# Kernel optimization log

Hardware: AMD Instinct MI355X
Metric: run time of the kernel (lower is better)

## Reference

```python
import jax, jax.numpy as jnp
import numpy as np

# ---- module config (from init_kwargs) ----
KERNEL_SIZE = 3
DIM = 3
HALF = KERNEL_SIZE // 2          # kernel offsets span [-HALF, HALF]
COORD_RANGE = 256                # voxel grid extent per spatial axis
NUM_BATCH = 4
N_VOXELS = 100_000
FEAT_DIM = 32
STRIDE = COORD_RANGE + 2 * HALF  # encoding stride so shifted coords fit


def _kernel_offsets():
    # All offsets of a KERNEL_SIZE^DIM kernel, centered (MinkowskiEngine-style).
    r = np.arange(-HALF, HALF + 1)
    grids = np.meshgrid(*([r] * DIM), indexing='ij')
    return jnp.asarray(np.stack([g.ravel() for g in grids], axis=1), dtype=jnp.int32)  # [K, DIM]


def setup_inputs() -> dict:
    key = jax.random.key(0)
    k1, k2, k3 = jax.random.split(key, 3)
    batch = jax.random.randint(k1, (1, N_VOXELS), 0, NUM_BATCH, dtype=jnp.int32)
    coords = jax.random.randint(k2, (3, N_VOXELS), 0, COORD_RANGE, dtype=jnp.int32)
    sparse_indices = jnp.concatenate([batch, coords], axis=0)  # [4, N]
    features = jax.random.normal(k3, (N_VOXELS, FEAT_DIM), dtype=jnp.float32)
    return {"sparse_indices": sparse_indices, "features": features}


def _kernel_map_and_out_key(sparse_indices):
    offsets = _kernel_offsets()                 # [K, 3]
    K = offsets.shape[0]
    b = sparse_indices[0].astype(jnp.int32)     # [N]
    coords = sparse_indices[1:].T.astype(jnp.int32)  # [N, 3]
    N = coords.shape[0]
    NK = N * K

    # neighbor coords per (voxel, offset); shift by HALF so values are >= 0
    nbr = coords[:, None, :] + offsets[None, :, :] + HALF     # [N, K, 3]
    S = STRIDE
    # unique integer hash of (batch, x, y, z); fits in int32 for these ranges
    enc = ((b[:, None] * S + nbr[..., 0]) * S + nbr[..., 1]) * S + nbr[..., 2]
    enc = enc.reshape(-1)                                     # [NK]

    # unique keys (sorted) + inverse map; pad to static size NK
    uniq, inv = jnp.unique(enc, return_inverse=True, size=NK, fill_value=-1)

    # reorder unique keys into first-seen order to match the dict-based reference
    first = jnp.full((NK,), NK, dtype=jnp.int32).at[inv].min(
        jnp.arange(NK, dtype=jnp.int32))
    order = jnp.argsort(first)                                # padding sorts last
    new_id = jnp.zeros((NK,), dtype=jnp.int32).at[order].set(
        jnp.arange(NK, dtype=jnp.int32))
    out_idx = new_id[inv]                                     # [NK] output index per entry

    # decode unique (first-seen ordered) keys back to spatial coords
    uo = uniq[order]
    valid = uo >= 0
    z = uo % S
    y = (uo // S) % S
    x = (uo // (S * S)) % S
    out_key = jnp.stack([x, y, z], axis=1) - HALF             # undo shift
    out_key = jnp.where(valid[:, None], out_key, -1)          # [NK, 3], padded rows = -1

    input_idx = jnp.repeat(jnp.arange(N, dtype=jnp.int32), K) # [NK]
    rel_pos = jnp.tile(jnp.arange(K, dtype=jnp.int32), N)     # [NK]
    kernel_map = jnp.stack([input_idx, out_idx, rel_pos], axis=1)  # [NK, 3]
    return kernel_map, out_key


def reference(sparse_indices, features):
    kernel_map, out_key = _kernel_map_and_out_key(sparse_indices)
    NK = kernel_map.shape[0]
    # canonical downstream use of the kernel map: gather inputs, scatter-sum to outputs
    out_feats = jax.ops.segment_sum(features[kernel_map[:, 0]],
                                    kernel_map[:, 1], num_segments=NK)
    return kernel_map, out_key, out_feats
```

## Files before the change

### kernel.cpp

```cpp
#include <hip/hip_runtime.h>
#include <stdint.h>

typedef unsigned long long u64;
typedef unsigned u32;
typedef float __attribute__((ext_vector_type(4))) f4raw;

#define K 27
#define S 258
#define ENCMAX (4 * S * S * S)

struct __align__(16) BP { u64 bits; u32 pfx; u32 pad; };

__global__ void k_mark(const int* __restrict__ si, int N, u64* __restrict__ bits) {
    int idx = blockIdx.x * blockDim.x + threadIdx.x;
    if (idx >= N * 9) return;
    int n = idx / 9, run = idx - n * 9;
    int ox = run / 3, oy = run - ox * 3;
    int b = si[n], x = si[N + n], y = si[2 * N + n], z = si[3 * N + n];
    unsigned enc0 = (unsigned)(((b * S + x + ox) * S + (y + oy)) * S + z);
    unsigned w = enc0 >> 6; int bit = enc0 & 63;
    atomicOr(&bits[w], 7ull << bit);
    if (bit > 61) atomicOr(&bits[w + 1], 7ull >> (64 - bit));
}

__global__ void s1_tilesum(const u64* __restrict__ bits, int* __restrict__ tsums) {
    __shared__ int s[256];
    int tid = threadIdx.x;
    const u64* p = bits + (size_t)blockIdx.x * 4096;
    int sum = 0;
    for (int j = tid; j < 4096; j += 256) sum += __popcll(p[j]);
    s[tid] = sum; __syncthreads();
    for (int off = 128; off > 0; off >>= 1) {
        if (tid < off) s[tid] += s[tid + off];
        __syncthreads();
    }
    if (tid == 0) tsums[blockIdx.x] = s[0];
}

__global__ void k_scanB(int* __restrict__ a, int n) {
    __shared__ int s[1024];
    int tid = threadIdx.x;
    int v = (tid < n) ? a[tid] : 0;
    s[tid] = v; __syncthreads();
    for (int off = 1; off < 1024; off <<= 1) {
        int t = (tid >= off) ? s[tid - off] : 0;
        __syncthreads();
        s[tid] += t;
        __syncthreads();
    }
    if (tid == 1023) a[n] = s[1023];
    if (tid < n) a[tid] = s[tid] - v;
}

__global__ void s3_wprefix(const u64* __restrict__ bits, const int* __restrict__ tsums,
                           BP* __restrict__ bpx) {
    __shared__ int s[256];
    int tid = threadIdx.x;
    size_t base = (size_t)blockIdx.x * 4096 + (size_t)tid * 16;
    u64 wv[16]; int pc[16]; int tsum = 0;
#pragma unroll
    for (int j = 0; j < 16; j++) {
        wv[j] = bits[base + j];
        pc[j] = __popcll(wv[j]);
        tsum += pc[j];
    }
    s[tid] = tsum; __syncthreads();
    for (int off = 1; off < 256; off <<= 1) {
        int t = (tid >= off) ? s[tid - off] : 0;
        __syncthreads();
        s[tid] += t;
        __syncthreads();
    }
    int run = tsums[blockIdx.x] + s[tid] - tsum;
#pragma unroll
    for (int j = 0; j < 16; j++) {
        BP r; r.bits = wv[j]; r.pfx = (u32)run; r.pad = 0;
        bpx[base + j] = r;
        run += pc[j];
    }
}

__global__ void k_kid(const int* __restrict__ si, int N,
                      const BP* __restrict__ bpx,
                      int* __restrict__ kid, int* __restrict__ minE) {
    int idx = blockIdx.x * blockDim.x + threadIdx.x;
    if (idx >= N * 9) return;
    int n = idx / 9, run = idx - n * 9;
    int ox = run / 3, oy = run - ox * 3;
    int b = si[n], x = si[N + n], y = si[2 * N + n], z = si[3 * N + n];
    unsigned enc0 = (unsigned)(((b * S + x + ox) * S + (y + oy)) * S + z);
    int e0 = n * K + run * 3;
    unsigned w = enc0 >> 6; int bit = enc0 & 63;
    BP r = bpx[w];
    int kd0 = (int)r.pfx + __popcll(r.bits & ((1ull << bit) - 1));
    kid[e0 + 0] = kd0;
    kid[e0 + 1] = kd0 + 1;
    kid[e0 + 2] = kd0 + 2;
    atomicMin(&minE[kd0 + 0], e0 + 0);
    atomicMin(&minE[kd0 + 1], e0 + 1);
    atomicMin(&minE[kd0 + 2], e0 + 2);
}

__global__ void k_flagsum(const int* __restrict__ kid, const int* __restrict__ minE,
                          int NK, u32* __restrict__ multibk,
                          u64* __restrict__ flagw, int* __restrict__ bsums) {
    __shared__ int s[256];
    int tid = threadIdx.x;
    int tilebase = blockIdx.x * 4096;
    int sum = 0;
#pragma unroll
    for (int j = 0; j < 16; j++) {
        int e = tilebase + j * 256 + tid;
        int f = 0;
        if (e < NK) {
            int kd = kid[e];
            if (minE[kd] == e) f = 1;
            else atomicOr(&multibk[kd >> 5], 1u << (kd & 31));
        }
        u64 b = __ballot(f);
        if ((tid & 63) == 0) flagw[(unsigned)e >> 6] = b;
        sum += f;
    }
    s[tid] = sum; __syncthreads();
    for (int off = 128; off > 0; off >>= 1) {
        if (tid < off) s[tid] += s[tid + off];
        __syncthreads();
    }
    if (tid == 0) bsums[blockIdx.x] = s[0];
}

__global__ void k_scanC(const int* __restrict__ kid, const u64* __restrict__ flagw,
                        const int* __restrict__ bsums, const int* __restrict__ si,
                        const u32* __restrict__ multibk, int N, int NK, int NB,
                        float* __restrict__ out_key, int* __restrict__ rank_key,
                        float4* __restrict__ outF4) {
    __shared__ int s[256];
    int tid = threadIdx.x;
    int base = blockIdx.x * 4096 + tid * 16;
    int kv[16];
    *(int4*)(kv + 0)  = *(const int4*)(kid + base + 0);
    *(int4*)(kv + 4)  = *(const int4*)(kid + base + 4);
    *(int4*)(kv + 8)  = *(const int4*)(kid + base + 8);
    *(int4*)(kv + 12) = *(const int4*)(kid + base + 12);
    u64 word = flagw[(unsigned)base >> 6];
    int fbits = (int)((word >> ((tid & 3) * 16)) & 0xFFFFu);
    int tsum = __popc(fbits);
    s[tid] = tsum; __syncthreads();
    for (int off = 1; off < 256; off <<= 1) {
        int t = (tid >= off) ? s[tid - off] : 0;
        __syncthreads();
        s[tid] += t;
        __syncthreads();
    }
    int offset = bsums[blockIdx.x] + s[tid] - tsum;
    float4 zf = {0.f, 0.f, 0.f, 0.f};
    int run = 0;
#pragma unroll
    for (int j = 0; j < 16; j++) {
        int e = base + j;
        int f = (fbits >> j) & 1;
        if (f) {
            int rank = offset + run;
            int n = e / K; int m = e - n * K;
            int x = si[N + n], y = si[2 * N + n], z = si[3 * N + n];
            int ox = m / 9; int rm = m - ox * 9; int oy = rm / 3; int oz = rm - oy * 3;
            out_key[(size_t)rank * 3 + 0] = (float)(x + ox - 1);
            out_key[(size_t)rank * 3 + 1] = (float)(y + oy - 1);
            out_key[(size_t)rank * 3 + 2] = (float)(z + oz - 1);
            int kd = kv[j];
            rank_key[kd] = rank;
            if ((multibk[kd >> 5] >> (kd & 31)) & 1) {
                float4* q = outF4 + (size_t)rank * 8;
#pragma unroll
                for (int q8 = 0; q8 < 8; q8++) q[q8] = zf;
            }
        }
        run += f;
    }
    int U = bsums[NB];
    int rows = NK - U;
    int gs = gridDim.x * blockDim.x;
    for (int i = blockIdx.x * blockDim.x + tid; i < rows; i += gs) {
        int row = U + i;
        float4* q = outF4 + (size_t)row * 8;
#pragma unroll
        for (int q8 = 0; q8 < 8; q8++) q[q8] = zf;
        out_key[(size_t)row * 3 + 0] = -1.0f;
        out_key[(size_t)row * 3 + 1] = -1.0f;
        out_key[(size_t)row * 3 + 2] = -1.0f;
    }
}

__global__ void k_final(const int* __restrict__ kid, const int* __restrict__ rank_key,
                        const u32* __restrict__ multibk,
                        const float4* __restrict__ feat4,
                        float* __restrict__ km, float* __restrict__ outF, int NK) {
    int idx = blockIdx.x * blockDim.x + threadIdx.x;
    if (idx >= NK * 8) return;
    int e = idx >> 3, g = idx & 7;
    int kd = kid[e];
    int uid = rank_key[kd];
    int multi = (multibk[kd >> 5] >> (kd & 31)) & 1;
    int n = e / K, m = e - n * K;
    float4 v = feat4[(size_t)n * 8 + g];
    float* dst = outF + (size_t)uid * 32 + g * 4;
    if (multi) {
        atomicAdd(dst + 0, v.x);
        atomicAdd(dst + 1, v.y);
        atomicAdd(dst + 2, v.z);
        atomicAdd(dst + 3, v.w);
    } else {
        f4raw vr = {v.x, v.y, v.z, v.w};
        __builtin_nontemporal_store(vr, (f4raw*)dst);
    }
    if (g < 3)
        km[(size_t)e * 3 + g] = (g == 0) ? (float)n
                               : ((g == 1) ? (float)uid : (float)m);
}

extern "C" void kernel_launch(void* const* d_in, const int* in_sizes, int n_in,
                              void* d_out, int out_size, void* d_ws, size_t ws_size,
                              hipStream_t stream) {
    const int* si = (const int*)d_in[0];
    const float4* feat4 = (const float4*)d_in[1];
    int N = in_sizes[0] / 4;
    int NK = N * K;
    int NKp = (NK + 4095) & ~4095;
    int NB = NKp / 4096;
    int nkw = (NK + 31) / 32;

    int NW = (ENCMAX + 63) / 64;
    int NT = (NW + 4095) / 4096;
    int NWp = NT * 4096;

    float* km = (float*)d_out;
    float* out_key = km + (size_t)NK * 3;
    float* outF = km + (size_t)NK * 6;

    char* w = (char*)d_ws;
    char* p_bits    = w; w += ((size_t)NWp * 8 + 15) & ~(size_t)15;
    char* p_multibk = w; w += ((size_t)nkw * 4 + 15) & ~(size_t)15;
    size_t zbytes   = (size_t)(w - (char*)d_ws);
    char* p_tsums   = w; w += ((size_t)(NT + 1) * 4 + 15) & ~(size_t)15;
    char* p_bpx     = w; w += ((size_t)NWp * 16 + 15) & ~(size_t)15;
    char* p_minE    = w; w += ((size_t)NK * 4 + 15) & ~(size_t)15;
    char* p_kid     = w; w += ((size_t)NKp * 4 + 15) & ~(size_t)15;
    char* p_rank    = w; w += ((size_t)NK * 4 + 15) & ~(size_t)15;
    char* p_flagw   = w; w += ((size_t)(NKp / 64) * 8 + 15) & ~(size_t)15;
    char* p_bsums   = w; w += ((size_t)(NB + 1) * 4 + 15) & ~(size_t)15;

    u64* bits     = (u64*)p_bits;
    u32* multibk  = (u32*)p_multibk;
    int* tsums    = (int*)p_tsums;
    BP*  bpx      = (BP*)p_bpx;
    int* minE     = (int*)p_minE;
    int* kid      = (int*)p_kid;
    int* rank_key = (int*)p_rank;
    u64* flagw    = (u64*)p_flagw;
    int* bsums    = (int*)p_bsums;

    (void)hipMemsetAsync(d_ws, 0, zbytes, stream);
    (void)hipMemsetAsync(minE, 0x7F, (size_t)NK * 4, stream);

    int nb9 = (N * 9 + 255) / 256;
    k_mark<<<nb9, 256, 0, stream>>>(si, N, bits);
    s1_tilesum<<<NT, 256, 0, stream>>>(bits, tsums);
    k_scanB<<<1, 1024, 0, stream>>>(tsums, NT);
    s3_wprefix<<<NT, 256, 0, stream>>>(bits, tsums, bpx);
    k_kid<<<nb9, 256, 0, stream>>>(si, N, bpx, kid, minE);
    k_flagsum<<<NB, 256, 0, stream>>>(kid, minE, NK, multibk, flagw, bsums);
    k_scanB<<<1, 1024, 0, stream>>>(bsums, NB);
    k_scanC<<<NB, 256, 0, stream>>>(kid, flagw, bsums, si, multibk, N, NK, NB,
                                    out_key, rank_key, (float4*)outF);
    k_final<<<(NK * 8 + 255) / 256, 256, 0, stream>>>(kid, rank_key, multibk,
                                                      feat4, km, outF, NK);
}
```

Baseline: 699.9 us.

## Remove single-block scan launches, fold minE init into mark, compress kid storage

Drops the two single-block k_scanB launches. Each consuming block now recomputes its own tile prefix by reducing the preceding tile sums (s3_wprefix) or block sums (k_scanC), which also gives k_scanC the grand total. The minE memset is folded into k_mark as a grid-stride fill, and kid is stored once per 3-wide z-run (kid3) with the other two entries derived from it, cutting that buffer's writes and reads to a third. This costs redundant prefix reductions that grow with block index, plus extra integer divisions by 3 in the later kernels.

```diff
diff --git a/kernel.cpp b/kernel.cpp
--- a/kernel.cpp
+++ b/kernel.cpp
@@ -11,8 +11,11 @@
 
 struct __align__(16) BP { u64 bits; u32 pfx; u32 pad; };
 
-__global__ void k_mark(const int* __restrict__ si, int N, u64* __restrict__ bits) {
+__global__ void k_mark(const int* __restrict__ si, int N, int NK,
+                       u64* __restrict__ bits, int* __restrict__ minE) {
     int idx = blockIdx.x * blockDim.x + threadIdx.x;
+    int gs = gridDim.x * blockDim.x;
+    for (int i = idx; i < NK; i += gs) minE[i] = 0x7FFFFFFF;
     if (idx >= N * 9) return;
     int n = idx / 9, run = idx - n * 9;
     int ox = run / 3, oy = run - ox * 3;
@@ -37,25 +40,19 @@
     if (tid == 0) tsums[blockIdx.x] = s[0];
 }
 
-__global__ void k_scanB(int* __restrict__ a, int n) {
-    __shared__ int s[1024];
-    int tid = threadIdx.x;
-    int v = (tid < n) ? a[tid] : 0;
-    s[tid] = v; __syncthreads();
-    for (int off = 1; off < 1024; off <<= 1) {
-        int t = (tid >= off) ? s[tid - off] : 0;
-        __syncthreads();
-        s[tid] += t;
-        __syncthreads();
-    }
-    if (tid == 1023) a[n] = s[1023];
-    if (tid < n) a[tid] = s[tid] - v;
-}
-
 __global__ void s3_wprefix(const u64* __restrict__ bits, const int* __restrict__ tsums,
-                           BP* __restrict__ bpx) {
-    __shared__ int s[256];
-    int tid = threadIdx.x;
+                           int NT, BP* __restrict__ bpx) {
+    __shared__ int s[256];
+    int tid = threadIdx.x;
+    int part = 0;
+    for (int i = tid; i < blockIdx.x; i += 256) part += tsums[i];
+    s[tid] = part; __syncthreads();
+    for (int off = 128; off > 0; off >>= 1) {
+        if (tid < off) s[tid] += s[tid + off];
+        __syncthreads();
+    }
+    int tile_pfx = s[0];
+    __syncthreads();
     size_t base = (size_t)blockIdx.x * 4096 + (size_t)tid * 16;
     u64 wv[16]; int pc[16]; int tsum = 0;
 #pragma unroll
@@ -71,7 +68,7 @@
         s[tid] += t;
         __syncthreads();
     }
-    int run = tsums[blockIdx.x] + s[tid] - tsum;
+    int run = tile_pfx + s[tid] - tsum;
 #pragma unroll
     for (int j = 0; j < 16; j++) {
         BP r; r.bits = wv[j]; r.pfx = (u32)run; r.pad = 0;
@@ -82,7 +79,7 @@
 
 __global__ void k_kid(const int* __restrict__ si, int N,
                       const BP* __restrict__ bpx,
-                      int* __restrict__ kid, int* __restrict__ minE) {
+                      int* __restrict__ kid3, int* __restrict__ minE) {
     int idx = blockIdx.x * blockDim.x + threadIdx.x;
     if (idx >= N * 9) return;
     int n = idx / 9, run = idx - n * 9;
@@ -93,15 +90,13 @@
     unsigned w = enc0 >> 6; int bit = enc0 & 63;
     BP r = bpx[w];
     int kd0 = (int)r.pfx + __popcll(r.bits & ((1ull << bit) - 1));
-    kid[e0 + 0] = kd0;
-    kid[e0 + 1] = kd0 + 1;
-    kid[e0 + 2] = kd0 + 2;
+    kid3[idx] = kd0;
     atomicMin(&minE[kd0 + 0], e0 + 0);
     atomicMin(&minE[kd0 + 1], e0 + 1);
     atomicMin(&minE[kd0 + 2], e0 + 2);
 }
 
-__global__ void k_flagsum(const int* __restrict__ kid, const int* __restrict__ minE,
+__global__ void k_flagsum(const int* __restrict__ kid3, const int* __restrict__ minE,
                           int NK, u32* __restrict__ multibk,
                           u64* __restrict__ flagw, int* __restrict__ bsums) {
     __shared__ int s[256];
@@ -113,7 +108,8 @@
         int e = tilebase + j * 256 + tid;
         int f = 0;
         if (e < NK) {
-            int kd = kid[e];
+            int e3 = e / 3;
+            int kd = kid3[e3] + (e - e3 * 3);
             if (minE[kd] == e) f = 1;
             else atomicOr(&multibk[kd >> 5], 1u << (kd & 31));
         }
@@ -129,19 +125,36 @@
     if (tid == 0) bsums[blockIdx.x] = s[0];
 }
 
-__global__ void k_scanC(const int* __restrict__ kid, const u64* __restrict__ flagw,
+__global__ void k_scanC(const int* __restrict__ kid3, const u64* __restrict__ flagw,
                         const int* __restrict__ bsums, const int* __restrict__ si,
                         const u32* __restrict__ multibk, int N, int NK, int NB,
                         float* __restrict__ out_key, int* __restrict__ rank_key,
                         float4* __restrict__ outF4) {
     __shared__ int s[256];
-    int tid = threadIdx.x;
+    __shared__ int sh_pfx, sh_tot;
+    int tid = threadIdx.x;
+    int pfx = 0, tot = 0;
+    for (int i = tid; i < NB; i += 256) {
+        int v = bsums[i];
+        tot += v;
+        if (i < blockIdx.x) pfx += v;
+    }
+    s[tid] = pfx; __syncthreads();
+    for (int off = 128; off > 0; off >>= 1) {
+        if (tid < off) s[tid] += s[tid + off];
+        __syncthreads();
+    }
+    if (tid == 0) sh_pfx = s[0];
+    __syncthreads();
+    s[tid] = tot; __syncthreads();
+    for (int off = 128; off > 0; off >>= 1) {
+        if (tid < off) s[tid] += s[tid + off];
+        __syncthreads();
+    }
+    if (tid == 0) sh_tot = s[0];
+    __syncthreads();
+
     int base = blockIdx.x * 4096 + tid * 16;
-    int kv[16];
-    *(int4*)(kv + 0)  = *(const int4*)(kid + base + 0);
-    *(int4*)(kv + 4)  = *(const int4*)(kid + base + 4);
-    *(int4*)(kv + 8)  = *(const int4*)(kid + base + 8);
-    *(int4*)(kv + 12) = *(const int4*)(kid + base + 12);
     u64 word = flagw[(unsigned)base >> 6];
     int fbits = (int)((word >> ((tid & 3) * 16)) & 0xFFFFu);
     int tsum = __popc(fbits);
@@ -152,7 +165,7 @@
         s[tid] += t;
         __syncthreads();
     }
-    int offset = bsums[blockIdx.x] + s[tid] - tsum;
+    int offset = sh_pfx + s[tid] - tsum;
     float4 zf = {0.f, 0.f, 0.f, 0.f};
     int run = 0;
 #pragma unroll
@@ -167,7 +180,8 @@
             out_key[(size_t)rank * 3 + 0] = (float)(x + ox - 1);
             out_key[(size_t)rank * 3 + 1] = (float)(y + oy - 1);
             out_key[(size_t)rank * 3 + 2] = (float)(z + oz - 1);
-            int kd = kv[j];
+            int e3 = e / 3;
+            int kd = kid3[e3] + (e - e3 * 3);
             rank_key[kd] = rank;
             if ((multibk[kd >> 5] >> (kd & 31)) & 1) {
                 float4* q = outF4 + (size_t)rank * 8;
@@ -177,7 +191,7 @@
         }
         run += f;
     }
-    int U = bsums[NB];
+    int U = sh_tot;
     int rows = NK - U;
     int gs = gridDim.x * blockDim.x;
     for (int i = blockIdx.x * blockDim.x + tid; i < rows; i += gs) {
@@ -191,14 +205,15 @@
     }
 }
 
-__global__ void k_final(const int* __restrict__ kid, const int* __restrict__ rank_key,
+__global__ void k_final(const int* __restrict__ kid3, const int* __restrict__ rank_key,
                         const u32* __restrict__ multibk,
                         const float4* __restrict__ feat4,
                         float* __restrict__ km, float* __restrict__ outF, int NK) {
     int idx = blockIdx.x * blockDim.x + threadIdx.x;
     if (idx >= NK * 8) return;
     int e = idx >> 3, g = idx & 7;
-    int kd = kid[e];
+    int e3 = e / 3;
+    int kd = kid3[e3] + (e - e3 * 3);
     int uid = rank_key[kd];
     int multi = (multibk[kd >> 5] >> (kd & 31)) & 1;
     int n = e / K, m = e - n * K;
@@ -244,7 +259,7 @@
     char* p_tsums   = w; w += ((size_t)(NT + 1) * 4 + 15) & ~(size_t)15;
     char* p_bpx     = w; w += ((size_t)NWp * 16 + 15) & ~(size_t)15;
     char* p_minE    = w; w += ((size_t)NK * 4 + 15) & ~(size_t)15;
-    char* p_kid     = w; w += ((size_t)NKp * 4 + 15) & ~(size_t)15;
+    char* p_kid3    = w; w += ((size_t)(N * 9 + 2048) * 4 + 15) & ~(size_t)15;
     char* p_rank    = w; w += ((size_t)NK * 4 + 15) & ~(size_t)15;
     char* p_flagw   = w; w += ((size_t)(NKp / 64) * 8 + 15) & ~(size_t)15;
     char* p_bsums   = w; w += ((size_t)(NB + 1) * 4 + 15) & ~(size_t)15;
@@ -254,24 +269,21 @@
     int* tsums    = (int*)p_tsums;
     BP*  bpx      = (BP*)p_bpx;
     int* minE     = (int*)p_minE;
-    int* kid      = (int*)p_kid;
+    int* kid3     = (int*)p_kid3;
     int* rank_key = (int*)p_rank;
     u64* flagw    = (u64*)p_flagw;
     int* bsums    = (int*)p_bsums;
 
     (void)hipMemsetAsync(d_ws, 0, zbytes, stream);
-    (void)hipMemsetAsync(minE, 0x7F, (size_t)NK * 4, stream);
 
     int nb9 = (N * 9 + 255) / 256;
-    k_mark<<<nb9, 256, 0, stream>>>(si, N, bits);
+    k_mark<<<nb9, 256, 0, stream>>>(si, N, NK, bits, minE);
     s1_tilesum<<<NT, 256, 0, stream>>>(bits, tsums);
-    k_scanB<<<1, 1024, 0, stream>>>(tsums, NT);
-    s3_wprefix<<<NT, 256, 0, stream>>>(bits, tsums, bpx);
-    k_kid<<<nb9, 256, 0, stream>>>(si, N, bpx, kid, minE);
-    k_flagsum<<<NB, 256, 0, stream>>>(kid, minE, NK, multibk, flagw, bsums);
-    k_scanB<<<1, 1024, 0, stream>>>(bsums, NB);
-    k_scanC<<<NB, 256, 0, stream>>>(kid, flagw, bsums, si, multibk, N, NK, NB,
+    s3_wprefix<<<NT, 256, 0, stream>>>(bits, tsums, NT, bpx);
+    k_kid<<<nb9, 256, 0, stream>>>(si, N, bpx, kid3, minE);
+    k_flagsum<<<NB, 256, 0, stream>>>(kid3, minE, NK, multibk, flagw, bsums);
+    k_scanC<<<NB, 256, 0, stream>>>(kid3, flagw, bsums, si, multibk, N, NK, NB,
                                     out_key, rank_key, (float4*)outF);
-    k_final<<<(NK * 8 + 255) / 256, 256, 0, stream>>>(kid, rank_key, multibk,
+    k_final<<<(NK * 8 + 255) / 256, 256, 0, stream>>>(kid3, rank_key, multibk,
                                                       feat4, km, outF, NK);
 }
```

Result: no change. 702.9 us (+0.4%).
